# Kernel optimization log

Hardware: AMD Instinct MI355X
Metric: run time of the kernel (lower is better)

## Reference

```python
import jax, jax.numpy as jnp
import numpy as np

N_SRC = 50000
N_DST = 50000
N_EDGES = 1_600_000
D_NEIGH = 128
D_SELF = 128
D_EDGE = 32
D_OUT = 256


def setup_inputs() -> dict:
    key = jax.random.key(0)
    k = jax.random.split(key, 7)
    h_neigh = jax.random.normal(k[0], (N_SRC, D_NEIGH), dtype=jnp.float32)
    h_self = jax.random.normal(k[1], (N_DST, D_SELF), dtype=jnp.float32)
    edge_feats = jax.random.normal(k[2], (N_EDGES, D_EDGE), dtype=jnp.float32)
    src = jax.random.randint(k[3], (N_EDGES,), 0, N_SRC, dtype=jnp.int32)
    dst = jax.random.randint(k[4], (N_EDGES,), 0, N_DST, dtype=jnp.int32)
    # xavier-ish small weights
    W_self = jax.random.normal(k[5], (D_OUT, D_SELF), dtype=jnp.float32) * 0.05
    W_neigh = jax.random.normal(k[6], (D_OUT, D_NEIGH + D_EDGE), dtype=jnp.float32) * 0.05
    return {"h_neigh": h_neigh, "h_self": h_self, "edge_feats": edge_feats,
            "src": src, "dst": dst, "W_self": W_self, "W_neigh": W_neigh}


def reference(h_neigh, h_self, edge_feats, src, dst, W_self, W_neigh):
    n_dst = h_self.shape[0]
    # in-degree per destination node (mean denominator); zero-degree -> 0 result like DGL
    deg = jax.ops.segment_sum(jnp.ones_like(dst, dtype=h_neigh.dtype), dst, num_segments=n_dst)
    denom = jnp.where(deg == 0, 1.0, deg)[:, None]
    # fn.copy_e + mean: mean of edge features per destination node
    edge_agg = jax.ops.segment_sum(edge_feats, dst, num_segments=n_dst) / denom  # [n_dst, D_EDGE]
    # fn.copy_u + mean: gather neighbor features along edges, mean-scatter to dst
    neigh_agg = jax.ops.segment_sum(h_neigh[src], dst, num_segments=n_dst) / denom  # [n_dst, D_NEIGH]
    hn = jnp.concatenate([neigh_agg, edge_agg], axis=1)  # [n_dst, D_NEIGH+D_EDGE]
    z = jax.nn.relu(h_self @ W_self.T + hn @ W_neigh.T)  # [n_dst, D_OUT]
    z_norm = jnp.linalg.norm(z, ord=2, axis=1, keepdims=True)
    z_norm = jnp.where(z_norm == 0, 1.0, z_norm)
    return z / z_norm
```

## Files before the change

kernel.cpp:

```cpp
#include <hip/hip_runtime.h>

#define N_SRC 50000
#define N_DST 50000
#define N_EDGES 1600000
#define D_NEIGH 128
#define D_SELF 128
#define D_EDGE 32
#define D_OUT 256
#define K_TOT 288
#define D_HN 160

#define NBF 782
#define CPAD 16
#define CHUNK 2048
#define CAPSH 12
#define NSCAT1 256

typedef float f32x4 __attribute__((ext_vector_type(4)));
typedef short s16x8 __attribute__((ext_vector_type(8)));
typedef float fv4 __attribute__((ext_vector_type(4)));
typedef float fv2 __attribute__((ext_vector_type(2)));
typedef unsigned short uv4 __attribute__((ext_vector_type(4)));

__device__ __forceinline__ ushort f2bf(float x) {
    unsigned b = __float_as_uint(x);
    return (ushort)((b + 0x7fffu + ((b >> 16) & 1u)) >> 16);
}


#if defined(__has_builtin)
#if __has_builtin(__builtin_amdgcn_cvt_pk_fp8_f32) && __has_builtin(__builtin_amdgcn_cvt_pk_f32_fp8)
#define FP8_HW 1
#endif
#endif

__device__ __forceinline__ unsigned enc_fp8_scalar(float x) {
    unsigned b = __float_as_uint(x);
    const unsigned s = b >> 31;
    float ax = fabsf(x);
    ax = fminf(ax, 448.f);
    if (ax < 0.015625f) return s << 7;
    unsigned ab = __float_as_uint(ax);
    unsigned lsb = (ab >> 20) & 1u;
    unsigned b2 = ab + 0x7FFFFu + lsb;
    unsigned e = ((b2 >> 23) & 0xFFu) - 120u;
    unsigned m = (b2 >> 20) & 7u;
    if (e > 15u) { e = 15u; m = 6u; }
    return (s << 7) | (e << 3) | m;
}

__device__ __forceinline__ unsigned enc_fp8x4(float4 f) {
#ifdef FP8_HW
    int r = 0;
    r = __builtin_amdgcn_cvt_pk_fp8_f32(f.x, f.y, r, false);
    r = __builtin_amdgcn_cvt_pk_fp8_f32(f.z, f.w, r, true);
    return (unsigned)r;
#else
    return enc_fp8_scalar(f.x) | (enc_fp8_scalar(f.y) << 8) |
           (enc_fp8_scalar(f.z) << 16) | (enc_fp8_scalar(f.w) << 24);
#endif
}

__device__ __forceinline__ float dec_fp8_scalar(unsigned u) {
    unsigned e = (u >> 3) & 15u;
    unsigned bits = ((u & 0x80u) << 24) | (((u & 0x7Fu) << 20) + (120u << 23));
    return (e == 0) ? 0.f : __uint_as_float(bits);
}

__device__ __forceinline__ void dec_fp8x4(unsigned u, float* f) {
#ifdef FP8_HW
    fv2 lo = __builtin_amdgcn_cvt_pk_f32_fp8(u, false);
    fv2 hi = __builtin_amdgcn_cvt_pk_f32_fp8(u, true);
    f[0] = lo.x; f[1] = lo.y; f[2] = hi.x; f[3] = hi.y;
#else
    f[0] = dec_fp8_scalar(u);
    f[1] = dec_fp8_scalar(u >> 8);
    f[2] = dec_fp8_scalar(u >> 16);
    f[3] = dec_fp8_scalar(u >> 24);
#endif
}


__global__ __launch_bounds__(256) void k_pre(const int* __restrict__ dst,
                                             const int* __restrict__ src,
                                             int* __restrict__ gcur0,
                                             int2* __restrict__ pk1,
                                             const float* __restrict__ h_neigh,
                                             unsigned* __restrict__ hb,
                                             const float* __restrict__ h_self,
                                             ushort* __restrict__ hsb,
                                             const float* __restrict__ Wself,
                                             const float* __restrict__ Wneigh,
                                             ushort* __restrict__ Wb) {
    __shared__ int hist[NBF];
    __shared__ int lbase[NBF];
    __shared__ int gbase[NBF];
    __shared__ int partial[256];
    __shared__ int2 stage[CHUNK];
    const int blk = blockIdx.x;
    const int tid = threadIdx.x;

    if (blk >= NSCAT1) {
        const int bb = blk - NSCAT1;
        if (bb < 6250) {
            const int i = bb * 256 + tid;
            float4 f = ((const float4*)h_neigh)[i];
            hb[i] = enc_fp8x4(f);
        } else if (bb < 12500) {
            const int i = (bb - 6250) * 256 + tid;
            float4 f = ((const float4*)h_self)[i];
            ((ushort4*)hsb)[i] = make_ushort4(f2bf(f.x), f2bf(f.y), f2bf(f.z), f2bf(f.w));
        } else {
            const int q = (bb - 12500) * 256 + tid;
            if (q >= 9 * 4 * 256) return;
            const int t = q >> 10;
            const int r = q & 1023;
            const int k8 = r >> 8;
            const int c = r & 255;
            const int kb = t * 32 + k8 * 8;
            const float* p = (kb < 128) ? (Wself + (size_t)c * D_SELF + kb)
                                        : (Wneigh + (size_t)c * D_HN + (kb - 128));
            float4 f0 = *(const float4*)(p);
            float4 f1 = *(const float4*)(p + 4);
            ushort* o = Wb + (size_t)q * 8;
            *(ushort4*)(o)     = make_ushort4(f2bf(f0.x), f2bf(f0.y), f2bf(f0.z), f2bf(f0.w));
            *(ushort4*)(o + 4) = make_ushort4(f2bf(f1.x), f2bf(f1.y), f2bf(f1.z), f2bf(f1.w));
        }
        return;
    }

    const int n = N_EDGES;
    for (int c0 = blk * CHUNK; c0 < n; c0 += NSCAT1 * CHUNK) {
        const int m = min(CHUNK, n - c0);
        for (int t = tid; t < NBF; t += 256) hist[t] = 0;
        __syncthreads();
        int d8[8], s8[8];
#pragma unroll
        for (int j = 0; j < 8; j++) {
            const int i = c0 + j * 256 + tid;
            if (i < n) { d8[j] = dst[i]; s8[j] = src[i]; atomicAdd(&hist[d8[j] >> 6], 1); }
        }
        __syncthreads();
        int loc[4];
        int sum = 0;
#pragma unroll
        for (int j = 0; j < 4; j++) {
            const int bi = tid * 4 + j;
            loc[j] = (bi < NBF) ? hist[bi] : 0;
            sum += loc[j];
        }
        partial[tid] = sum;
        __syncthreads();
        for (int off = 1; off < 256; off <<= 1) {
            int v = (tid >= off) ? partial[tid - off] : 0;
            __syncthreads();
            partial[tid] += v;
            __syncthreads();
        }
        int ex = (tid == 0) ? 0 : partial[tid - 1];
#pragma unroll
        for (int j = 0; j < 4; j++) {
            const int bi = tid * 4 + j;
            if (bi < NBF) { lbase[bi] = ex; ex += loc[j]; }
        }
        __syncthreads();
        for (int t = tid; t < NBF; t += 256)
            gbase[t] = hist[t] ? atomicAdd(&gcur0[t * CPAD], hist[t]) : 0;
        __syncthreads();
        for (int t = tid; t < NBF; t += 256) hist[t] = lbase[t];
        __syncthreads();
#pragma unroll
        for (int j = 0; j < 8; j++) {
            const int i = c0 + j * 256 + tid;
            if (i < n) {
                const unsigned cb = (unsigned)d8[j] >> 6;
                const int p = atomicAdd(&hist[cb], 1);
                stage[p] = make_int2(i, (int)((unsigned)s8[j] |
                                              (((unsigned)d8[j] & 63u) << 16) | (cb << 22)));
            }
        }
        __syncthreads();
        for (int t = tid; t < m; t += 256) {
            int2 v = stage[t];
            const unsigned cb = ((unsigned)v.y >> 22) & 1023u;
            v.y &= 0x3FFFFF;
            pk1[((size_t)cb << CAPSH) + gbase[cb] + (t - lbase[cb])] = v;
        }
        __syncthreads();
    }
}


__global__ __launch_bounds__(512) void k_aggs2(const int* __restrict__ gcur0,
                                               const int2* __restrict__ pk1,
                                               const unsigned char* __restrict__ hb,
                                               const float* __restrict__ ef,
                                               ushort* __restrict__ hnb) {
    __shared__ int2 sorted[1 << CAPSH];
    __shared__ int h[64];
    __shared__ int sbase[65];
    __shared__ int cur[64];
    const int b = blockIdx.x;
    const int tid = threadIdx.x;
    const int lane = tid & 63;
    const int wid = tid >> 6;
    const int nn = min(gcur0[b * CPAD], 1 << CAPSH);
    const size_t base = (size_t)b << CAPSH;

    if (tid < 64) h[tid] = 0;
    __syncthreads();

    int2 ent[8];
    int ne = 0;
#pragma unroll
    for (int j = 0; j < 8; j++) {
        const int idx = j * 512 + tid;
        if (idx < nn) {
            unsigned long long pv =
                __builtin_nontemporal_load((const unsigned long long*)&pk1[base + idx]);
            ent[ne].x = (int)(unsigned)pv;
            ent[ne].y = (int)(unsigned)(pv >> 32);
            atomicAdd(&h[(ent[ne].y >> 16) & 63], 1);
            ne++;
        }
    }
    __syncthreads();
    if (tid < 64) {
        const int v = h[tid];
        int p = v;
#pragma unroll
        for (int off = 1; off < 64; off <<= 1) {
            int q = __shfl_up(p, off);
            if (lane >= off) p += q;
        }
        sbase[tid + 1] = p;
        if (tid == 0) sbase[0] = 0;
        cur[tid] = p - v;
    }
    __syncthreads();
    for (int j = 0; j < ne; j++) {
        const int dl = (ent[j].y >> 16) & 63;
        const int p = atomicAdd(&cur[dl], 1);
        sorted[p] = make_int2(ent[j].x, ent[j].y & 0xFFFF);
    }
    __syncthreads();

    const int g = lane >> 5;
    const int ll = lane & 31;
    const unsigned char* hbase = hb + 4 * ll;
    const float* ebase = ef + ll;

    for (int r = 0; r < 8; r++) {
        const int dl = wid * 8 + r;
        const int gn = b * 64 + dl;
        const int start = sbase[dl], end = sbase[dl + 1];
        const int deg = end - start;
        float a0 = 0.f, a1 = 0.f, a2 = 0.f, a3 = 0.f, ae = 0.f;

        for (int c = start; c < end; c += 64) {
            const int rem = end - c;
            const int m = rem < 64 ? rem : 64;
            int e = 0, s = 0;
            if (lane < m) { int2 p = sorted[c + lane]; e = p.x; s = p.y; }
            int i = 0;
            for (; i + 16 <= m; i += 16) {
                unsigned u[8];
                float te[8];
#pragma unroll
                for (int j = 0; j < 8; j++) {
                    const int sj = __shfl(s, i + 2 * j + g);
                    u[j] = *(const unsigned*)(hbase + (size_t)sj * D_NEIGH);
                }
#pragma unroll
                for (int j = 0; j < 8; j++) {
                    const int ee = __shfl(e, i + 2 * j + g);
                    te[j] = __builtin_nontemporal_load(ebase + (size_t)ee * D_EDGE);
                }
#pragma unroll
                for (int j = 0; j < 8; j++) {
                    float f[4];
                    dec_fp8x4(u[j], f);
                    a0 += f[0]; a1 += f[1]; a2 += f[2]; a3 += f[3];
                    ae += te[j];
                }
            }
            for (; i + 8 <= m; i += 8) {
                unsigned u[4];
                float te[4];
#pragma unroll
                for (int j = 0; j < 4; j++) {
                    const int sj = __shfl(s, i + 2 * j + g);
                    u[j] = *(const unsigned*)(hbase + (size_t)sj * D_NEIGH);
                }
#pragma unroll
                for (int j = 0; j < 4; j++) {
                    const int ee = __shfl(e, i + 2 * j + g);
                    te[j] = __builtin_nontemporal_load(ebase + (size_t)ee * D_EDGE);
                }
#pragma unroll
                for (int j = 0; j < 4; j++) {
                    float f[4];
                    dec_fp8x4(u[j], f);
                    a0 += f[0]; a1 += f[1]; a2 += f[2]; a3 += f[3];
                    ae += te[j];
                }
            }
            for (; i < m; ++i) {
                const int si = __builtin_amdgcn_readlane(s, i);
                const int ei = __builtin_amdgcn_readlane(e, i);
                if (g == 0) {
                    const unsigned uu = *(const unsigned*)(hbase + (size_t)si * D_NEIGH);
                    float f[4];
                    dec_fp8x4(uu, f);
                    a0 += f[0]; a1 += f[1]; a2 += f[2]; a3 += f[3];
                    ae += __builtin_nontemporal_load(ebase + (size_t)ei * D_EDGE);
                }
            }
        }

        a0 += __shfl_xor(a0, 32); a1 += __shfl_xor(a1, 32);
        a2 += __shfl_xor(a2, 32); a3 += __shfl_xor(a3, 32);
        ae += __shfl_xor(ae, 32);

        if (gn < N_DST && lane < 32) {
            const float inv = 1.0f / (float)(deg > 0 ? deg : 1);
            ushort* o = hnb + (size_t)gn * D_HN;
            *(ushort4*)(o + 4 * ll) = make_ushort4(f2bf(a0 * inv), f2bf(a1 * inv),
                                                   f2bf(a2 * inv), f2bf(a3 * inv));
            o[128 + ll] = f2bf(ae * inv);
        }
    }
}


#define GBM 128

__global__ __launch_bounds__(512) void k_gemm_norm(const ushort* __restrict__ hsb,
                                                   const ushort* __restrict__ hnb,
                                                   const ushort* __restrict__ Wb,
                                                   float* __restrict__ out) {
    __shared__ __align__(16) ushort Xs[2][GBM * 40];
    __shared__ float rsum[2][GBM];
    __shared__ float invn[GBM];

    const int tid = threadIdx.x;
    const int lane = tid & 63;
    const int wid = tid >> 6;
    const int wm = wid >> 1;
    const int wn = wid & 1;
    const int brow = blockIdx.x * GBM;
    const int xrow = tid >> 2, xpart = tid & 3;
    const int koff8 = lane >> 4, rsel = lane & 15;

    f32x4 acc[2][8] = {};

    auto stageX = [&](int t, int bufi) {
        const int k0 = t * 32;
        const int gr = brow + xrow;
        uv4 v0 = (uv4)0, v1 = (uv4)0;
        if (gr < N_DST) {
            const ushort* sp = (k0 < 128) ? (hsb + (size_t)gr * D_SELF + k0 + xpart * 8)
                                          : (hnb + (size_t)gr * D_HN + (k0 - 128) + xpart * 8);
            v0 = __builtin_nontemporal_load((const uv4*)(sp));
            v1 = __builtin_nontemporal_load((const uv4*)(sp + 4));
        }
        *(uv4*)&Xs[bufi][xrow * 40 + xpart * 8] = v0;
        *(uv4*)&Xs[bufi][xrow * 40 + xpart * 8 + 4] = v1;
    };

    stageX(0, 0);
    __syncthreads();

    for (int t = 0; t < 9; t++) {
        if (t < 8) stageX(t + 1, (t + 1) & 1);
        s16x8 af[2], bf[8];
#pragma unroll
        for (int fi = 0; fi < 2; fi++)
            af[fi] = *(const s16x8*)&Xs[t & 1][(wm * 32 + fi * 16 + rsel) * 40 + koff8 * 8];
#pragma unroll
        for (int fj = 0; fj < 8; fj++)
            bf[fj] = *(const s16x8*)&Wb[((size_t)(t * 4 + koff8) * 256 +
                                         (wn * 128 + fj * 16 + rsel)) * 8];
#pragma unroll
        for (int fi = 0; fi < 2; fi++)
#pragma unroll
            for (int fj = 0; fj < 8; fj++)
                acc[fi][fj] = __builtin_amdgcn_mfma_f32_16x16x32_bf16(af[fi], bf[fj], acc[fi][fj], 0, 0, 0);
        __syncthreads();
    }

    float ss[2][4];
#pragma unroll
    for (int fi = 0; fi < 2; fi++)
#pragma unroll
        for (int j = 0; j < 4; j++) {
            float s = 0.f;
#pragma unroll
            for (int fj = 0; fj < 8; fj++) {
                float z = fmaxf(acc[fi][fj][j], 0.f);
                acc[fi][fj][j] = z;
                s += z * z;
            }
            ss[fi][j] = s;
        }
#pragma unroll
    for (int m = 1; m < 16; m <<= 1)
#pragma unroll
        for (int fi = 0; fi < 2; fi++)
#pragma unroll
            for (int j = 0; j < 4; j++) ss[fi][j] += __shfl_xor(ss[fi][j], m);
    if ((lane & 15) == 0) {
        const int gg = lane >> 4;
#pragma unroll
        for (int fi = 0; fi < 2; fi++)
#pragma unroll
            for (int j = 0; j < 4; j++)
                rsum[wn][wm * 32 + fi * 16 + gg * 4 + j] = ss[fi][j];
    }
    __syncthreads();
    if (tid < GBM) {
        float t = rsum[0][tid] + rsum[1][tid];
        invn[tid] = (t > 0.f) ? 1.f / sqrtf(t) : 1.f;
    }
    __syncthreads();

#pragma unroll
    for (int fi = 0; fi < 2; fi++)
#pragma unroll
        for (int j = 0; j < 4; j++) {
            const int rl = wm * 32 + fi * 16 + (lane >> 4) * 4 + j;
            const int row = brow + rl;
            if (row < N_DST) {
                const float iv = invn[rl];
#pragma unroll
                for (int fj = 0; fj < 8; fj++)
                    __builtin_nontemporal_store(acc[fi][fj][j] * iv,
                        &out[(size_t)row * D_OUT + wn * 128 + fj * 16 + (lane & 15)]);
            }
        }
}


extern "C" void kernel_launch(void* const* d_in, const int* in_sizes, int n_in,
                              void* d_out, int out_size, void* d_ws, size_t ws_size,
                              hipStream_t stream) {
    const float* h_neigh = (const float*)d_in[0];
    const float* h_self  = (const float*)d_in[1];
    const float* ef      = (const float*)d_in[2];
    const int*   src     = (const int*)d_in[3];
    const int*   dst     = (const int*)d_in[4];
    const float* Wself   = (const float*)d_in[5];
    const float* Wneigh  = (const float*)d_in[6];
    float* out = (float*)d_out;

    char* ws = (char*)d_ws;
    int*      gcur0 = (int*)(ws + 0);
    int2*     pk1   = (int2*)(ws + 65536);
    unsigned* hb    = (unsigned*)(ws + 25690112);
    ushort*   hsb   = (ushort*)(ws + 32090112);
    ushort*   hnb   = (ushort*)(ws + 44890112);
    ushort*   Wb    = (ushort*)(ws + 60890112);

    hipMemsetAsync(gcur0, 0, NBF * CPAD * sizeof(int), stream);
    k_pre<<<NSCAT1 + 6250 + 6250 + 36, 256, 0, stream>>>(dst, src, gcur0, pk1,
                                                         h_neigh, hb, h_self, hsb,
                                                         Wself, Wneigh, Wb);
    k_aggs2<<<NBF, 512, 0, stream>>>(gcur0, pk1, (const unsigned char*)hb, ef, hnb);
    k_gemm_norm<<<(N_DST + GBM - 1) / GBM, 512, 0, stream>>>(hsb, hnb, Wb, out);
}
```

Before: 163.8 us.

## Split fused sort+aggregate kernel into bucket-sort and per-node aggregation kernels

The single k_aggs2 kernel did the within-bucket sort in LDS and then aggregated 64 destination nodes per 512-thread block. This splits it into k_scat2, which writes the locally sorted edges to a global buffer pk2 along with per-node start/end ranges, and k_agg, which gives each wavefront one destination node in small 128-thread blocks. The aim is finer-grained scheduling and better load balance across the many uneven node degrees, plus lower LDS use for higher occupancy. The cost is an extra kernel launch and an extra global write and read of the sorted edge list.

Result: slower. 167.4 us (+2.2%).

```diff
diff --git a/kernel.cpp b/kernel.cpp
--- a/kernel.cpp
+++ b/kernel.cpp
@@ -18,7 +18,6 @@
 
 typedef float f32x4 __attribute__((ext_vector_type(4)));
 typedef short s16x8 __attribute__((ext_vector_type(8)));
-typedef float fv4 __attribute__((ext_vector_type(4)));
 typedef float fv2 __attribute__((ext_vector_type(2)));
 typedef unsigned short uv4 __attribute__((ext_vector_type(4)));
 
@@ -152,9 +151,9 @@
         partial[tid] = sum;
         __syncthreads();
         for (int off = 1; off < 256; off <<= 1) {
-            int v = (tid >= off) ? partial[tid - off] : 0;
+            int q = (tid >= off) ? partial[tid - off] : 0;
             __syncthreads();
-            partial[tid] += v;
+            partial[tid] += q;
             __syncthreads();
         }
         int ex = (tid == 0) ? 0 : partial[tid - 1];
@@ -181,48 +180,35 @@
         }
         __syncthreads();
         for (int t = tid; t < m; t += 256) {
-            int2 v = stage[t];
-            const unsigned cb = ((unsigned)v.y >> 22) & 1023u;
-            v.y &= 0x3FFFFF;
-            pk1[((size_t)cb << CAPSH) + gbase[cb] + (t - lbase[cb])] = v;
-        }
-        __syncthreads();
-    }
-}
-
-
-__global__ __launch_bounds__(512) void k_aggs2(const int* __restrict__ gcur0,
+            int2 v2 = stage[t];
+            const unsigned cb = ((unsigned)v2.y >> 22) & 1023u;
+            v2.y &= 0x3FFFFF;
+            pk1[((size_t)cb << CAPSH) + gbase[cb] + (t - lbase[cb])] = v2;
+        }
+        __syncthreads();
+    }
+}
+
+
+__global__ __launch_bounds__(256) void k_scat2(const int* __restrict__ gcur0,
                                                const int2* __restrict__ pk1,
-                                               const unsigned char* __restrict__ hb,
-                                               const float* __restrict__ ef,
-                                               ushort* __restrict__ hnb) {
-    __shared__ int2 sorted[1 << CAPSH];
+                                               int2* __restrict__ pk2,
+                                               int2* __restrict__ rs2) {
     __shared__ int h[64];
-    __shared__ int sbase[65];
     __shared__ int cur[64];
     const int b = blockIdx.x;
+    const int n = min(gcur0[b * CPAD], 1 << CAPSH);
+    const int base = b << CAPSH;
     const int tid = threadIdx.x;
-    const int lane = tid & 63;
-    const int wid = tid >> 6;
-    const int nn = min(gcur0[b * CPAD], 1 << CAPSH);
-    const size_t base = (size_t)b << CAPSH;
-
     if (tid < 64) h[tid] = 0;
     __syncthreads();
 
-    int2 ent[8];
+    int2 ent[16];
     int ne = 0;
-#pragma unroll
-    for (int j = 0; j < 8; j++) {
-        const int idx = j * 512 + tid;
-        if (idx < nn) {
-            unsigned long long pv =
-                __builtin_nontemporal_load((const unsigned long long*)&pk1[base + idx]);
-            ent[ne].x = (int)(unsigned)pv;
-            ent[ne].y = (int)(unsigned)(pv >> 32);
-            atomicAdd(&h[(ent[ne].y >> 16) & 63], 1);
-            ne++;
-        }
+    for (int i = tid; i < n; i += 256) {
+        ent[ne] = pk1[base + i];
+        atomicAdd(&h[(ent[ne].y >> 16) & 63], 1);
+        ne++;
     }
     __syncthreads();
     if (tid < 64) {
@@ -231,104 +217,114 @@
 #pragma unroll
         for (int off = 1; off < 64; off <<= 1) {
             int q = __shfl_up(p, off);
-            if (lane >= off) p += q;
-        }
-        sbase[tid + 1] = p;
-        if (tid == 0) sbase[0] = 0;
+            if (tid >= off) p += q;
+        }
         cur[tid] = p - v;
+        const int gn = b * 64 + tid;
+        if (gn < N_DST) rs2[gn] = make_int2(base + p - v, base + p);
     }
     __syncthreads();
     for (int j = 0; j < ne; j++) {
         const int dl = (ent[j].y >> 16) & 63;
         const int p = atomicAdd(&cur[dl], 1);
-        sorted[p] = make_int2(ent[j].x, ent[j].y & 0xFFFF);
-    }
-    __syncthreads();
-
+        pk2[base + p] = make_int2(ent[j].x, ent[j].y & 0xFFFF);
+    }
+}
+
+
+__global__ __launch_bounds__(128) void k_agg(const int2* __restrict__ rs2,
+                                             const int2* __restrict__ pk,
+                                             const unsigned char* __restrict__ hb,
+                                             const float* __restrict__ ef,
+                                             ushort* __restrict__ hnb) {
+    const int d = blockIdx.x * 2 + (threadIdx.x >> 6);
+    const int lane = threadIdx.x & 63;
+    if (d >= N_DST) return;
+    const int ll = lane & 31;
     const int g = lane >> 5;
-    const int ll = lane & 31;
+    const int2 se = rs2[d];
+    const int start = se.x, end = se.y;
+    const int deg = end - start;
+    float a0 = 0.f, a1 = 0.f, a2 = 0.f, a3 = 0.f, ae = 0.f;
     const unsigned char* hbase = hb + 4 * ll;
     const float* ebase = ef + ll;
 
-    for (int r = 0; r < 8; r++) {
-        const int dl = wid * 8 + r;
-        const int gn = b * 64 + dl;
-        const int start = sbase[dl], end = sbase[dl + 1];
-        const int deg = end - start;
-        float a0 = 0.f, a1 = 0.f, a2 = 0.f, a3 = 0.f, ae = 0.f;
-
-        for (int c = start; c < end; c += 64) {
-            const int rem = end - c;
-            const int m = rem < 64 ? rem : 64;
-            int e = 0, s = 0;
-            if (lane < m) { int2 p = sorted[c + lane]; e = p.x; s = p.y; }
-            int i = 0;
-            for (; i + 16 <= m; i += 16) {
-                unsigned u[8];
-                float te[8];
-#pragma unroll
-                for (int j = 0; j < 8; j++) {
-                    const int sj = __shfl(s, i + 2 * j + g);
-                    u[j] = *(const unsigned*)(hbase + (size_t)sj * D_NEIGH);
-                }
-#pragma unroll
-                for (int j = 0; j < 8; j++) {
-                    const int ee = __shfl(e, i + 2 * j + g);
-                    te[j] = __builtin_nontemporal_load(ebase + (size_t)ee * D_EDGE);
-                }
-#pragma unroll
-                for (int j = 0; j < 8; j++) {
-                    float f[4];
-                    dec_fp8x4(u[j], f);
-                    a0 += f[0]; a1 += f[1]; a2 += f[2]; a3 += f[3];
-                    ae += te[j];
-                }
-            }
-            for (; i + 8 <= m; i += 8) {
-                unsigned u[4];
-                float te[4];
-#pragma unroll
-                for (int j = 0; j < 4; j++) {
-                    const int sj = __shfl(s, i + 2 * j + g);
-                    u[j] = *(const unsigned*)(hbase + (size_t)sj * D_NEIGH);
-                }
-#pragma unroll
-                for (int j = 0; j < 4; j++) {
-                    const int ee = __shfl(e, i + 2 * j + g);
-                    te[j] = __builtin_nontemporal_load(ebase + (size_t)ee * D_EDGE);
-                }
-#pragma unroll
-                for (int j = 0; j < 4; j++) {
-                    float f[4];
-                    dec_fp8x4(u[j], f);
-                    a0 += f[0]; a1 += f[1]; a2 += f[2]; a3 += f[3];
-                    ae += te[j];
-                }
-            }
-            for (; i < m; ++i) {
-                const int si = __builtin_amdgcn_readlane(s, i);
-                const int ei = __builtin_amdgcn_readlane(e, i);
-                if (g == 0) {
-                    const unsigned uu = *(const unsigned*)(hbase + (size_t)si * D_NEIGH);
-                    float f[4];
-                    dec_fp8x4(uu, f);
-                    a0 += f[0]; a1 += f[1]; a2 += f[2]; a3 += f[3];
-                    ae += __builtin_nontemporal_load(ebase + (size_t)ei * D_EDGE);
-                }
-            }
-        }
-
-        a0 += __shfl_xor(a0, 32); a1 += __shfl_xor(a1, 32);
-        a2 += __shfl_xor(a2, 32); a3 += __shfl_xor(a3, 32);
-        ae += __shfl_xor(ae, 32);
-
-        if (gn < N_DST && lane < 32) {
-            const float inv = 1.0f / (float)(deg > 0 ? deg : 1);
-            ushort* o = hnb + (size_t)gn * D_HN;
-            *(ushort4*)(o + 4 * ll) = make_ushort4(f2bf(a0 * inv), f2bf(a1 * inv),
-                                                   f2bf(a2 * inv), f2bf(a3 * inv));
-            o[128 + ll] = f2bf(ae * inv);
-        }
+    for (int c = start; c < end; c += 64) {
+        const int rem = end - c;
+        const int m = rem < 64 ? rem : 64;
+        int e = 0, s = 0;
+        if (lane < m) {
+            unsigned long long pv =
+                __builtin_nontemporal_load((const unsigned long long*)&pk[c + lane]);
+            e = (int)(unsigned)pv;
+            s = (int)(unsigned)(pv >> 32);
+        }
+        int i = 0;
+        for (; i + 16 <= m; i += 16) {
+            unsigned u[8];
+            float te[8];
+#pragma unroll
+            for (int j = 0; j < 8; j++) {
+                const int sj = __shfl(s, i + 2 * j + g);
+                u[j] = *(const unsigned*)(hbase + (size_t)sj * D_NEIGH);
+            }
+#pragma unroll
+            for (int j = 0; j < 8; j++) {
+                const int ee = __shfl(e, i + 2 * j + g);
+                te[j] = __builtin_nontemporal_load(ebase + (size_t)ee * D_EDGE);
+            }
+#pragma unroll
+            for (int j = 0; j < 8; j++) {
+                float f[4];
+                dec_fp8x4(u[j], f);
+                a0 += f[0]; a1 += f[1]; a2 += f[2]; a3 += f[3];
+                ae += te[j];
+            }
+        }
+        for (; i + 8 <= m; i += 8) {
+            unsigned u[4];
+            float te[4];
+#pragma unroll
+            for (int j = 0; j < 4; j++) {
+                const int sj = __shfl(s, i + 2 * j + g);
+                u[j] = *(const unsigned*)(hbase + (size_t)sj * D_NEIGH);
+            }
+#pragma unroll
+            for (int j = 0; j < 4; j++) {
+                const int ee = __shfl(e, i + 2 * j + g);
+                te[j] = __builtin_nontemporal_load(ebase + (size_t)ee * D_EDGE);
+            }
+#pragma unroll
+            for (int j = 0; j < 4; j++) {
+                float f[4];
+                dec_fp8x4(u[j], f);
+                a0 += f[0]; a1 += f[1]; a2 += f[2]; a3 += f[3];
+                ae += te[j];
+            }
+        }
+        for (; i < m; ++i) {
+            const int si = __builtin_amdgcn_readlane(s, i);
+            const int ei = __builtin_amdgcn_readlane(e, i);
+            if (g == 0) {
+                const unsigned uu = *(const unsigned*)(hbase + (size_t)si * D_NEIGH);
+                float f[4];
+                dec_fp8x4(uu, f);
+                a0 += f[0]; a1 += f[1]; a2 += f[2]; a3 += f[3];
+                ae += __builtin_nontemporal_load(ebase + (size_t)ei * D_EDGE);
+            }
+        }
+    }
+
+    a0 += __shfl_xor(a0, 32); a1 += __shfl_xor(a1, 32);
+    a2 += __shfl_xor(a2, 32); a3 += __shfl_xor(a3, 32);
+    ae += __shfl_xor(ae, 32);
+
+    if (lane < 32) {
+        const float inv = 1.0f / (float)(deg > 0 ? deg : 1);
+        ushort* o = hnb + (size_t)d * D_HN;
+        *(ushort4*)(o + 4 * ll) = make_ushort4(f2bf(a0 * inv), f2bf(a1 * inv),
+                                               f2bf(a2 * inv), f2bf(a3 * inv));
+        o[128 + ll] = f2bf(ae * inv);
     }
 }
 
@@ -455,16 +451,19 @@
 
     char* ws = (char*)d_ws;
     int*      gcur0 = (int*)(ws + 0);
-    int2*     pk1   = (int2*)(ws + 65536);
-    unsigned* hb    = (unsigned*)(ws + 25690112);
-    ushort*   hsb   = (ushort*)(ws + 32090112);
-    ushort*   hnb   = (ushort*)(ws + 44890112);
-    ushort*   Wb    = (ushort*)(ws + 60890112);
+    int2*     rs2   = (int2*)(ws + 65536);
+    int2*     pk1   = (int2*)(ws + 524288);
+    int2*     pk2   = (int2*)(ws + 26148864);
+    unsigned* hb    = (unsigned*)(ws + 51773440);
+    ushort*   hsb   = (ushort*)(ws + 58173440);
+    ushort*   hnb   = (ushort*)(ws + 70973440);
+    ushort*   Wb    = (ushort*)(ws + 86973440);
 
     hipMemsetAsync(gcur0, 0, NBF * CPAD * sizeof(int), stream);
     k_pre<<<NSCAT1 + 6250 + 6250 + 36, 256, 0, stream>>>(dst, src, gcur0, pk1,
                                                          h_neigh, hb, h_self, hsb,
                                                          Wself, Wneigh, Wb);
-    k_aggs2<<<NBF, 512, 0, stream>>>(gcur0, pk1, (const unsigned char*)hb, ef, hnb);
+    k_scat2<<<NBF, 256, 0, stream>>>(gcur0, pk1, pk2, rs2);
+    k_agg<<<(N_DST + 1) / 2, 128, 0, stream>>>(rs2, pk2, (const unsigned char*)hb, ef, hnb);
     k_gemm_norm<<<(N_DST + GBM - 1) / GBM, 512, 0, stream>>>(hsb, hnb, Wb, out);
 }
```
